# Optimization experiments

Measured on AMD Instinct MI355X. Metric: run time of the kernel, lower is better.

Reference implementation:

```python
import jax, jax.numpy as jnp
import numpy as np

HEADS = 8
DIM_HEAD = 64
RMS_EPS = 1.1920929e-07  # torch default eps = finfo(fp32).eps


def rotate_half(x):
    x1, x2 = jnp.split(x, 2, axis=-1)
    return jnp.concatenate((-x2, x1), axis=-1)


def setup_inputs() -> dict:
    key = jax.random.key(0)
    k1, k2, k3, k4, k5 = jax.random.split(key, 5)
    b, n, dim = 2, 4096, 1024
    dim_hidden = HEADS * DIM_HEAD  # 512
    x = jax.random.normal(k1, (b, n, dim), dtype=jnp.float32)
    rotary_emb = jax.random.normal(k2, (n, DIM_HEAD), dtype=jnp.float32)
    rms_weight = jnp.ones((dim,), dtype=jnp.float32)
    w_qkv = jax.random.normal(k3, (dim, dim_hidden * 3), dtype=jnp.float32) * (dim ** -0.5)
    w_out = jax.random.normal(k4, (dim_hidden, dim), dtype=jnp.float32) * (dim_hidden ** -0.5)
    return {"x": x, "rotary_emb": rotary_emb, "rms_weight": rms_weight,
            "w_qkv": w_qkv, "w_out": w_out}


def reference(x, rotary_emb, rms_weight, w_qkv, w_out):
    b, n, dim = x.shape
    h, d = HEADS, DIM_HEAD
    # RMSNorm
    xn = x * jax.lax.rsqrt(jnp.mean(x * x, axis=-1, keepdims=True) + RMS_EPS) * rms_weight
    # QKV projection, rearrange 'b n (qkv h d) -> qkv b h n d'
    qkv = (xn @ w_qkv).reshape(b, n, 3, h, d).transpose(2, 0, 3, 1, 4)
    q, k, v = qkv[0], qkv[1], qkv[2]
    # RoPE
    cos, sin = jnp.cos(rotary_emb), jnp.sin(rotary_emb)  # (n, d) broadcasts over b,h
    q = q * cos + rotate_half(q) * sin
    k = k * cos + rotate_half(k) * sin
    q = q * (d ** -0.5)
    sim = jnp.einsum('bhid,bhjd->bhij', q, k)
    causal_mask = jnp.triu(jnp.ones((n, n), dtype=bool), 1)
    sim = jnp.where(causal_mask, -jnp.finfo(sim.dtype).max, sim)
    attn = jax.nn.softmax(sim, axis=-1)
    out = jnp.einsum('bhij,bhjd->bhid', attn, v)
    out = out.transpose(0, 2, 1, 3).reshape(b, n, h * d)  # 'b h n d -> b n (h d)'
    return out @ w_out
```

## Files before the change

### kernel.cpp

```cpp
#include <hip/hip_runtime.h>
#include <hip/hip_bf16.h>
#include <cstdint>

using bf16x8 = __attribute__((ext_vector_type(8))) __bf16;
using f32x4  = __attribute__((ext_vector_type(4))) float;

#define LOG2E 1.4426950408889634f

__device__ inline void gload16(__bf16* lds, const __bf16* g) {
    __builtin_amdgcn_global_load_lds((const __attribute__((address_space(1))) void*)g,
                                     (__attribute__((address_space(3))) void*)lds, 16, 0, 0);
}
__device__ inline void wait_barrier4() {
    asm volatile("s_waitcnt vmcnt(4)" ::: "memory");
    __builtin_amdgcn_s_barrier();
}
__device__ inline void wait_barrier0() {
    asm volatile("s_waitcnt vmcnt(0)" ::: "memory");
    __builtin_amdgcn_s_barrier();
}

__global__ __launch_bounds__(256) void prep_kernel(const float* __restrict__ x,
                                                   const float* __restrict__ rmsw,
                                                   __bf16* __restrict__ xn,
                                                   const float* __restrict__ wqkv,
                                                   __bf16* __restrict__ wqkvt,
                                                   const float* __restrict__ wout,
                                                   __bf16* __restrict__ woutt,
                                                   const float* __restrict__ rot,
                                                   uint* __restrict__ csb) {
    __shared__ float tile[32][33];
    __shared__ float part[4];
    const int bid = blockIdx.x;
    const int tid = threadIdx.x;
    if (bid < 8192) {
        const float4 v = reinterpret_cast<const float4*>(x + (size_t)bid * 1024)[tid];
        float ss = v.x * v.x + v.y * v.y + v.z * v.z + v.w * v.w;
#pragma unroll
        for (int i = 1; i < 64; i <<= 1) ss += __shfl_xor(ss, i);
        if ((tid & 63) == 0) part[tid >> 6] = ss;
        __syncthreads();
        const float total = part[0] + part[1] + part[2] + part[3];
        const float scale = rsqrtf(total * (1.0f / 1024.0f) + 1.1920929e-07f);
        const float4 wv = reinterpret_cast<const float4*>(rmsw)[tid];
        union { __bf16 h[4]; uint2 u; } pk;
        pk.h[0] = (__bf16)(v.x * scale * wv.x);
        pk.h[1] = (__bf16)(v.y * scale * wv.y);
        pk.h[2] = (__bf16)(v.z * scale * wv.z);
        pk.h[3] = (__bf16)(v.w * scale * wv.w);
        reinterpret_cast<uint2*>(xn + (size_t)bid * 1024)[tid] = pk.u;
    } else if (bid < 10240) {
        const float* in;
        __bf16* out;
        int K, N, bx, by;
        if (bid < 9728) {
            const int i = bid - 8192;
            in = wqkv; out = wqkvt; K = 1024; N = 1536; bx = i % 48; by = i / 48;
        } else {
            const int i = bid - 9728;
            in = wout; out = woutt; K = 512; N = 1024; bx = i % 32; by = i / 32;
        }
        const int tx = tid & 31, ty = tid >> 5;
        const int n0 = bx * 32, k0 = by * 32;
#pragma unroll
        for (int r = ty; r < 32; r += 8)
            tile[r][tx] = in[(size_t)(k0 + r) * N + n0 + tx];
        __syncthreads();
#pragma unroll
        for (int r = ty; r < 32; r += 8)
            out[(size_t)(n0 + r) * K + k0 + tx] = (__bf16)tile[tx][r];
    } else {
        const int i = (bid - 10240) * 256 + tid;
        float s, c;
        sincosf(rot[i], &s, &c);
        union { __bf16 h[2]; uint u; } p;
        p.h[0] = (__bf16)c;
        p.h[1] = (__bf16)s;
        csb[i] = p.u;
    }
}

__global__ __launch_bounds__(256) void rope_k_kernel(__bf16* __restrict__ qk,
                                                     const uint* __restrict__ csb) {
    const int row = blockIdx.x * 4 + (threadIdx.x >> 6);
    const int lane = threadIdx.x & 63;
    const int h = lane >> 3, dl = (lane & 7) * 4;
    const int pos = row & 4095;
    union { uint4 v; uint u[4]; } A, C;
    A.v = *reinterpret_cast<const uint4*>(csb + pos * 64 + dl);
    C.v = *reinterpret_cast<const uint4*>(csb + pos * 64 + dl + 32);
    __bf16* pp = qk + (size_t)row * 1024 + 512 + h * 64 + dl;
    union { uint2 u; __bf16 hh[4]; } va, vb, oa, ob;
    va.u = *reinterpret_cast<const uint2*>(pp);
    vb.u = *reinterpret_cast<const uint2*>(pp + 32);
#pragma unroll
    for (int j = 0; j < 4; ++j) {
        const float c0 = __uint_as_float(A.u[j] << 16);
        const float s0 = __uint_as_float(A.u[j] & 0xffff0000u);
        const float c1 = __uint_as_float(C.u[j] << 16);
        const float s1 = __uint_as_float(C.u[j] & 0xffff0000u);
        const float a = (float)va.hh[j], b2 = (float)vb.hh[j];
        oa.hh[j] = (__bf16)(a * c0 - b2 * s0);
        ob.hh[j] = (__bf16)(b2 * c1 + a * s1);
    }
    *reinterpret_cast<uint2*>(pp)      = oa.u;
    *reinterpret_cast<uint2*>(pp + 32) = ob.u;
}

__global__ __launch_bounds__(256) void gemm_qkv(const __bf16* __restrict__ A,
                                                const __bf16* __restrict__ Bt,
                                                __bf16* __restrict__ qk,
                                                __bf16* __restrict__ vt) {
    __shared__ __align__(16) __bf16 As[3][128 * 32];
    __shared__ __align__(16) __bf16 Bs[3][128 * 32];
    const int K = 1024, nbn = 12;
    const int xcd = blockIdx.x & 7;
    const int idx = blockIdx.x >> 3;
    const int bm = xcd * 8 + idx / nbn;
    const int bn = idx % nbn;
    const int tid = threadIdx.x;
    const int w = tid >> 6, l = tid & 63, lg = l >> 4, lr = l & 15;
    const int wr = w >> 1, wc = w & 1;
    const __bf16* Ab = A + (size_t)(bm * 128) * K;
    const __bf16* Bb = Bt + (size_t)(bn * 128) * K;
    const int srow = tid >> 2, scol = (tid & 3) * 8;
    const __bf16* Asrc = Ab + (size_t)srow * K + scol;
    const __bf16* Bsrc = Bb + (size_t)srow * K + scol;

    auto stage = [&](int k2) {
        const int nx = k2 % 3;
        const int off = k2 * 32;
        gload16(&As[nx][tid * 8],        Asrc + off);
        gload16(&As[nx][2048 + tid * 8], Asrc + (size_t)64 * K + off);
        gload16(&Bs[nx][tid * 8],        Bsrc + off);
        gload16(&Bs[nx][2048 + tid * 8], Bsrc + (size_t)64 * K + off);
    };

    const int NS = K >> 5;
    f32x4 acc[4][4] = {};
    stage(0);
    stage(1);
    wait_barrier4();

    if (bn < 8) {
        for (int k = 0; k < NS; ++k) {
            const bool more = (k + 2 < NS);
            if (more) stage(k + 2);
            const __bf16* Ac = &As[k % 3][0];
            const __bf16* Bc = &Bs[k % 3][0];
            bf16x8 af[4], bfr[4];
#pragma unroll
            for (int m = 0; m < 4; ++m)
                af[m] = *reinterpret_cast<const bf16x8*>(Ac + (wr * 64 + m * 16 + lr) * 32 + lg * 8);
#pragma unroll
            for (int nn = 0; nn < 4; ++nn)
                bfr[nn] = *reinterpret_cast<const bf16x8*>(Bc + (wc * 64 + nn * 16 + lr) * 32 + lg * 8);
#pragma unroll
            for (int m = 0; m < 4; ++m)
#pragma unroll
                for (int nn = 0; nn < 4; ++nn)
                    acc[m][nn] = __builtin_amdgcn_mfma_f32_16x16x32_bf16(bfr[m], af[nn],
                                                                         acc[m][nn], 0, 0, 0);
            if (more) wait_barrier4();
            else      wait_barrier0();
        }
        const int cb = bn * 128 + wc * 64;
#pragma unroll
        for (int m = 0; m < 4; ++m) {
            const int col = cb + m * 16 + 4 * lg;
#pragma unroll
            for (int nn = 0; nn < 4; ++nn) {
                const int row = bm * 128 + wr * 64 + nn * 16 + lr;
                union { __bf16 h4[4]; uint2 u; } ob;
#pragma unroll
                for (int r = 0; r < 4; ++r) ob.h4[r] = (__bf16)acc[m][nn][r];
                *reinterpret_cast<uint2*>(qk + (size_t)row * 1024 + col) = ob.u;
            }
        }
    } else {
        for (int k = 0; k < NS; ++k) {
            const bool more = (k + 2 < NS);
            if (more) stage(k + 2);
            const __bf16* Ac = &As[k % 3][0];
            const __bf16* Bc = &Bs[k % 3][0];
            bf16x8 af[4], bfr[4];
#pragma unroll
            for (int m = 0; m < 4; ++m)
                af[m] = *reinterpret_cast<const bf16x8*>(Ac + (wr * 64 + m * 16 + lr) * 32 + lg * 8);
#pragma unroll
            for (int nn = 0; nn < 4; ++nn)
                bfr[nn] = *reinterpret_cast<const bf16x8*>(Bc + (wc * 64 + nn * 16 + lr) * 32 + lg * 8);
#pragma unroll
            for (int m = 0; m < 4; ++m)
#pragma unroll
                for (int nn = 0; nn < 4; ++nn)
                    acc[m][nn] = __builtin_amdgcn_mfma_f32_16x16x32_bf16(af[m], bfr[nn],
                                                                         acc[m][nn], 0, 0, 0);
            if (more) wait_barrier4();
            else      wait_barrier0();
        }
        const int cb = bn * 128 + wc * 64;
#pragma unroll
        for (int m = 0; m < 4; ++m) {
            const int rg = bm * 128 + wr * 64 + m * 16 + 4 * lg;
            const int bidx = rg >> 12, pos0 = rg & 4095;
            const int a0 = pos0 & 63;
            const int cp = 32 * (a0 >> 5) + 8 * ((a0 >> 2) & 3) + 4 * ((a0 >> 4) & 1);
            const int nbase = (pos0 & ~63) + cp;
#pragma unroll
            for (int nn = 0; nn < 4; ++nn) {
                const int col = cb + nn * 16 + lr - 1024;
                const int hh = col >> 6, dd = col & 63;
                union { __bf16 h4[4]; uint2 u; } pk2;
#pragma unroll
                for (int r = 0; r < 4; ++r) pk2.h4[r] = (__bf16)acc[m][nn][r];
                *reinterpret_cast<uint2*>(&vt[((size_t)(bidx * 8 + hh) * 64 + dd) * 4096 + nbase]) = pk2.u;
            }
        }
    }
}

__global__ __launch_bounds__(256) void gemm_out(const __bf16* __restrict__ A,
                                                const __bf16* __restrict__ Bt,
                                                float* __restrict__ C) {
    __shared__ __align__(16) __bf16 As[3][128 * 32];
    __shared__ __align__(16) __bf16 Bs[3][128 * 32];
    const int K = 512, N = 1024, nbn = 8;
    const int xcd = blockIdx.x & 7;
    const int idx = blockIdx.x >> 3;
    const int bm = xcd * 8 + idx / nbn;
    const int bn = idx % nbn;
    const int tid = threadIdx.x;
    const int w = tid >> 6, l = tid & 63, lg = l >> 4, lr = l & 15;
    const int wr = w >> 1, wc = w & 1;
    const __bf16* Ab = A + (size_t)(bm * 128) * K;
    const __bf16* Bb = Bt + (size_t)(bn * 128) * K;
    const int srow = tid >> 2, scol = (tid & 3) * 8;
    const __bf16* Asrc = Ab + (size_t)srow * K + scol;
    const __bf16* Bsrc = Bb + (size_t)srow * K + scol;

    auto stage = [&](int k2) {
        const int nx = k2 % 3;
        const int off = k2 * 32;
        gload16(&As[nx][tid * 8],        Asrc + off);
        gload16(&As[nx][2048 + tid * 8], Asrc + (size_t)64 * K + off);
        gload16(&Bs[nx][tid * 8],        Bsrc + off);
        gload16(&Bs[nx][2048 + tid * 8], Bsrc + (size_t)64 * K + off);
    };

    const int NS = K >> 5;
    f32x4 acc[4][4] = {};
    stage(0);
    stage(1);
    wait_barrier4();
    for (int k = 0; k < NS; ++k) {
        const bool more = (k + 2 < NS);
        if (more) stage(k + 2);
        const __bf16* Ac = &As[k % 3][0];
        const __bf16* Bc = &Bs[k % 3][0];
        bf16x8 af[4], bfr[4];
#pragma unroll
        for (int m = 0; m < 4; ++m)
            af[m] = *reinterpret_cast<const bf16x8*>(Ac + (wr * 64 + m * 16 + lr) * 32 + lg * 8);
#pragma unroll
        for (int nn = 0; nn < 4; ++nn)
            bfr[nn] = *reinterpret_cast<const bf16x8*>(Bc + (wc * 64 + nn * 16 + lr) * 32 + lg * 8);
#pragma unroll
        for (int m = 0; m < 4; ++m)
#pragma unroll
            for (int nn = 0; nn < 4; ++nn)
                acc[m][nn] = __builtin_amdgcn_mfma_f32_16x16x32_bf16(bfr[m], af[nn],
                                                                     acc[m][nn], 0, 0, 0);
        if (more) wait_barrier4();
        else      wait_barrier0();
    }
#pragma unroll
    for (int m = 0; m < 4; ++m) {
        const int col = bn * 128 + wc * 64 + m * 16 + 4 * lg;
#pragma unroll
        for (int nn = 0; nn < 4; ++nn) {
            const int row = bm * 128 + wr * 64 + nn * 16 + lr;
            *reinterpret_cast<float4*>(&C[(size_t)row * N + col]) =
                *reinterpret_cast<const float4*>(&acc[m][nn]);
        }
    }
}

__global__ __launch_bounds__(256) void attn_kernel(const __bf16* __restrict__ qkp,
                                                   const __bf16* __restrict__ vt,
                                                   const uint* __restrict__ csb,
                                                   __bf16* __restrict__ attn_out) {
    const int bid = blockIdx.x;
    const int j = bid >> 3;
    const int bh = 2 * (bid & 7) + (j & 1);
    const int qt = 63 - (j >> 1);
    const int b = bh >> 3, h = bh & 7;
    const int tid = threadIdx.x;
    const int w = tid >> 6, l = tid & 63, lg = l >> 4, lr = l & 15;

    __shared__ __align__(16) __bf16 Ks[2][64 * 64];
    __shared__ __align__(16) __bf16 Vs[3][64 * 64];

    const __bf16* qbase = qkp + (size_t)b * 4096 * 1024 + h * 64;
    const __bf16* kbase = qbase + 512;
    const __bf16* vtb   = vt + (size_t)(b * 8 + h) * 64 * 4096;

    const int sr = tid >> 3;
    const int sc = ((tid & 7) ^ (sr & 7)) * 8;
    const __bf16* kp = kbase + (size_t)sr * 1024 + sc;
    const __bf16* vp = vtb + (size_t)sr * 4096 + sc;

    const int xel = (lr & 7) * 8;

    const int wq0 = qt * 64 + 16 * w;
    const int nkt = qt + 1;

    auto stage2 = [&](__bf16* kdst, __bf16* vdst) {
        gload16(kdst + tid * 8,         kp);
        gload16(kdst + (tid + 256) * 8, kp + 32 * 1024);
        gload16(vdst + tid * 8,         vp);
        gload16(vdst + (tid + 256) * 8, vp + 32 * 4096);
        kp += 64 * 1024;
        vp += 64;
    };

    stage2(Ks[0], Vs[0]);
    stage2(Ks[1], Vs[1]);

    bf16x8 Qf[2];
    {
        const __bf16* qp = qbase + (size_t)(wq0 + lr) * 1024 + 8 * lg;
        const bf16x8 rq0 = *reinterpret_cast<const bf16x8*>(qp);
        const bf16x8 rq1 = *reinterpret_cast<const bf16x8*>(qp + 32);
        const uint* csp = csb + (size_t)(wq0 + lr) * 64 + 8 * lg;
        union { uint4 q[2]; uint u[8]; } W0, W1;
        W0.q[0] = *reinterpret_cast<const uint4*>(csp);
        W0.q[1] = *reinterpret_cast<const uint4*>(csp + 4);
        W1.q[0] = *reinterpret_cast<const uint4*>(csp + 32);
        W1.q[1] = *reinterpret_cast<const uint4*>(csp + 36);
        const float qs = 0.125f * LOG2E;
#pragma unroll
        for (int i = 0; i < 8; ++i) {
            const float cax = __uint_as_float(W0.u[i] << 16);
            const float cay = __uint_as_float(W0.u[i] & 0xffff0000u);
            const float cbx = __uint_as_float(W1.u[i] << 16);
            const float cby = __uint_as_float(W1.u[i] & 0xffff0000u);
            const float a = (float)rq0[i], b2 = (float)rq1[i];
            Qf[0][i] = (__bf16)((a * cax - b2 * cay) * qs);
            Qf[1][i] = (__bf16)((b2 * cbx + a * cby) * qs);
        }
    }

    bf16x8 ones;
#pragma unroll
    for (int i = 0; i < 8; ++i) ones[i] = (__bf16)1.0f;

    f32x4 O[4] = {};
    f32x4 Lacc = {};
    float m_ = -1e30f;

    auto qk_step = [&](f32x4 (&S)[4], const __bf16* kb) {
        __builtin_amdgcn_s_setprio(1);
#pragma unroll
        for (int jt = 0; jt < 4; ++jt) {
            const __bf16* kr = kb + (16 * jt + lr) * 64;
            const bf16x8 Kf0 = *reinterpret_cast<const bf16x8*>(kr + ((8 * lg) ^ xel));
            const bf16x8 Kf1 = *reinterpret_cast<const bf16x8*>(kr + ((32 + 8 * lg) ^ xel));
            f32x4 z = {};
            z = __builtin_amdgcn_mfma_f32_16x16x32_bf16(Kf0, Qf[0], z, 0, 0, 0);
            S[jt] = __builtin_amdgcn_mfma_f32_16x16x32_bf16(Kf1, Qf[1], z, 0, 0, 0);
        }
        __builtin_amdgcn_s_setprio(0);
    };
    auto smpv = [&](f32x4 (&SC)[4], const __bf16* vb, bool domask) {
        if (domask) {
#pragma unroll
            for (int jt = 0; jt < 4; ++jt)
#pragma unroll
                for (int r = 0; r < 4; ++r)
                    if (16 * jt + 4 * lg + r > 16 * w + lr) SC[jt][r] = -1e30f;
        }
        float mx = -1e30f;
#pragma unroll
        for (int jt = 0; jt < 4; ++jt)
            mx = fmaxf(mx, fmaxf(fmaxf(SC[jt][0], SC[jt][1]), fmaxf(SC[jt][2], SC[jt][3])));
        if (__any(mx > m_ + 8.0f)) {
            mx = fmaxf(mx, __shfl_xor(mx, 16));
            mx = fmaxf(mx, __shfl_xor(mx, 32));
            const float mn = fmaxf(m_, mx);
            const float alpha = __builtin_amdgcn_exp2f(m_ - mn);
            m_ = mn;
            Lacc *= alpha;
#pragma unroll
            for (int dt = 0; dt < 4; ++dt) O[dt] *= alpha;
        }
#pragma unroll
        for (int jt = 0; jt < 4; ++jt)
#pragma unroll
            for (int r = 0; r < 4; ++r)
                SC[jt][r] = __builtin_amdgcn_exp2f(SC[jt][r] - m_);
        __builtin_amdgcn_s_setprio(1);
#pragma unroll
        for (int s = 0; s < 2; ++s) {
            bf16x8 Pf;
#pragma unroll
            for (int i = 0; i < 8; ++i)
                Pf[i] = (__bf16)SC[2 * s + (i >> 2)][i & 3];
            Lacc = __builtin_amdgcn_mfma_f32_16x16x32_bf16(ones, Pf, Lacc, 0, 0, 0);
#pragma unroll
            for (int dt = 0; dt < 4; ++dt) {
                const bf16x8 Vf = *reinterpret_cast<const bf16x8*>(
                    vb + (16 * dt + lr) * 64 + ((32 * s + 8 * lg) ^ xel));
                O[dt] = __builtin_amdgcn_mfma_f32_16x16x32_bf16(Vf, Pf, O[dt], 0, 0, 0);
            }
        }
        __builtin_amdgcn_s_setprio(0);
    };

    f32x4 S0[4], S1[4];
    int t = 0;

    __syncthreads();
    qk_step(S0, Ks[0]);
    __syncthreads();

    for (; t + 8 <= nkt; t += 6) {
        stage2(Ks[0], Vs[2]); qk_step(S1, Ks[1]); smpv(S0, Vs[0], false); __syncthreads();
        stage2(Ks[1], Vs[0]); qk_step(S0, Ks[0]); smpv(S1, Vs[1], false); __syncthreads();
        stage2(Ks[0], Vs[1]); qk_step(S1, Ks[1]); smpv(S0, Vs[2], false); __syncthreads();
        stage2(Ks[1], Vs[2]); qk_step(S0, Ks[0]); smpv(S1, Vs[0], false); __syncthreads();
        stage2(Ks[0], Vs[0]); qk_step(S1, Ks[1]); smpv(S0, Vs[1], false); __syncthreads();
        stage2(Ks[1], Vs[1]); qk_step(S0, Ks[0]); smpv(S1, Vs[2], false); __syncthreads();
    }

    {
        f32x4 Sp[4];
#pragma unroll
        for (int jt = 0; jt < 4; ++jt) Sp[jt] = S0[jt];
        for (; t < nkt; ++t) {
            if (t + 2 < nkt) stage2(Ks[(t + 2) & 1], Vs[(t + 2) % 3]);
            f32x4 Sn[4];
            if (t + 1 < nkt) qk_step(Sn, Ks[(t + 1) & 1]);
            smpv(Sp, Vs[t % 3], t == nkt - 1);
            __syncthreads();
#pragma unroll
            for (int jt = 0; jt < 4; ++jt) Sp[jt] = Sn[jt];
        }
    }

    const float inv = 1.0f / Lacc[0];
    __bf16* op = attn_out + ((size_t)b * 4096 + wq0 + lr) * 512 + h * 64;
#pragma unroll
    for (int dt = 0; dt < 4; ++dt) {
        union { __bf16 h4[4]; uint2 u; } ow;
#pragma unroll
        for (int r = 0; r < 4; ++r) ow.h4[r] = (__bf16)(O[dt][r] * inv);
        *reinterpret_cast<uint2*>(op + 16 * dt + 4 * lg) = ow.u;
    }
}

extern "C" void kernel_launch(void* const* d_in, const int* in_sizes, int n_in,
                              void* d_out, int out_size, void* d_ws, size_t ws_size,
                              hipStream_t stream) {
    (void)in_sizes; (void)n_in; (void)out_size; (void)ws_size;
    const float* x    = (const float*)d_in[0];
    const float* rot  = (const float*)d_in[1];
    const float* rmsw = (const float*)d_in[2];
    const float* wqkv = (const float*)d_in[3];
    const float* wout = (const float*)d_in[4];
    float* out = (float*)d_out;

    char* ws = (char*)d_ws;
    __bf16* xn    = (__bf16*)ws;
    __bf16* wqkvt = (__bf16*)(ws + 16777216);
    __bf16* woutt = (__bf16*)(ws + 16777216 + 3145728);
    __bf16* aout  = (__bf16*)(ws + 16777216 + 3145728 + 1048576);
    __bf16* qk  = (__bf16*)d_out;
    uint* csb   = (uint*)((char*)d_out + 16777216);
    __bf16* vt  = (__bf16*)((char*)d_out + 18874368);

    prep_kernel<<<11264, 256, 0, stream>>>(x, rmsw, xn, wqkv, wqkvt, wout, woutt, rot, csb);
    gemm_qkv<<<768, 256, 0, stream>>>(xn, wqkvt, qk, vt);
    rope_k_kernel<<<2048, 256, 0, stream>>>(qk, csb);
    attn_kernel<<<1024, 256, 0, stream>>>(qk, vt, csb, aout);
    gemm_out<<<512, 256, 0, stream>>>(aout, woutt, out);
}
```

Before: 130.4 us.

## Fuse RoPE and query scaling into QKV GEMM epilogue, drop rope kernel

Applies the rotary embedding to both Q and K, plus the softmax scale on Q, directly in the QKV GEMM epilogue. It pairs accumulator tiles m and m+2, which hold dims d and d+32 of the same head. This removes the separate rope_k kernel launch and its read-modify-write pass over K, and removes the per-block RoPE work on Q in the attention kernel. The cost is extra cos/sin table loads and arithmetic in the GEMM epilogue, and it depends on the tile-to-head column mapping being correct.

Measured after the change: 124.6 us. 4.4% less time.

```diff
diff --git a/kernel.cpp b/kernel.cpp
--- a/kernel.cpp
+++ b/kernel.cpp
@@ -80,35 +80,9 @@
     }
 }
 
-__global__ __launch_bounds__(256) void rope_k_kernel(__bf16* __restrict__ qk,
-                                                     const uint* __restrict__ csb) {
-    const int row = blockIdx.x * 4 + (threadIdx.x >> 6);
-    const int lane = threadIdx.x & 63;
-    const int h = lane >> 3, dl = (lane & 7) * 4;
-    const int pos = row & 4095;
-    union { uint4 v; uint u[4]; } A, C;
-    A.v = *reinterpret_cast<const uint4*>(csb + pos * 64 + dl);
-    C.v = *reinterpret_cast<const uint4*>(csb + pos * 64 + dl + 32);
-    __bf16* pp = qk + (size_t)row * 1024 + 512 + h * 64 + dl;
-    union { uint2 u; __bf16 hh[4]; } va, vb, oa, ob;
-    va.u = *reinterpret_cast<const uint2*>(pp);
-    vb.u = *reinterpret_cast<const uint2*>(pp + 32);
-#pragma unroll
-    for (int j = 0; j < 4; ++j) {
-        const float c0 = __uint_as_float(A.u[j] << 16);
-        const float s0 = __uint_as_float(A.u[j] & 0xffff0000u);
-        const float c1 = __uint_as_float(C.u[j] << 16);
-        const float s1 = __uint_as_float(C.u[j] & 0xffff0000u);
-        const float a = (float)va.hh[j], b2 = (float)vb.hh[j];
-        oa.hh[j] = (__bf16)(a * c0 - b2 * s0);
-        ob.hh[j] = (__bf16)(b2 * c1 + a * s1);
-    }
-    *reinterpret_cast<uint2*>(pp)      = oa.u;
-    *reinterpret_cast<uint2*>(pp + 32) = ob.u;
-}
-
 __global__ __launch_bounds__(256) void gemm_qkv(const __bf16* __restrict__ A,
                                                 const __bf16* __restrict__ Bt,
+                                                const uint* __restrict__ csb,
                                                 __bf16* __restrict__ qk,
                                                 __bf16* __restrict__ vt) {
     __shared__ __align__(16) __bf16 As[3][128 * 32];
@@ -165,16 +139,32 @@
             else      wait_barrier0();
         }
         const int cb = bn * 128 + wc * 64;
-#pragma unroll
-        for (int m = 0; m < 4; ++m) {
-            const int col = cb + m * 16 + 4 * lg;
-#pragma unroll
-            for (int nn = 0; nn < 4; ++nn) {
-                const int row = bm * 128 + wr * 64 + nn * 16 + lr;
-                union { __bf16 h4[4]; uint2 u; } ob;
-#pragma unroll
-                for (int r = 0; r < 4; ++r) ob.h4[r] = (__bf16)acc[m][nn][r];
-                *reinterpret_cast<uint2*>(qk + (size_t)row * 1024 + col) = ob.u;
+        const float sc = (cb < 512) ? 0.125f * LOG2E : 1.0f;
+#pragma unroll
+        for (int nn = 0; nn < 4; ++nn) {
+            const int row = bm * 128 + wr * 64 + nn * 16 + lr;
+            const int pos = row & 4095;
+            const uint* csp = csb + pos * 64 + 4 * lg;
+            __bf16* qrow = qk + (size_t)row * 1024 + cb + 4 * lg;
+#pragma unroll
+            for (int m = 0; m < 2; ++m) {
+                union { uint4 v; uint u[4]; } Wlo, Whi;
+                Wlo.v = *reinterpret_cast<const uint4*>(csp + m * 16);
+                Whi.v = *reinterpret_cast<const uint4*>(csp + m * 16 + 32);
+                union { __bf16 h4[4]; uint2 u; } lo, hi;
+#pragma unroll
+                for (int r = 0; r < 4; ++r) {
+                    const float c0 = __uint_as_float(Wlo.u[r] << 16);
+                    const float s0 = __uint_as_float(Wlo.u[r] & 0xffff0000u);
+                    const float c1 = __uint_as_float(Whi.u[r] << 16);
+                    const float s1 = __uint_as_float(Whi.u[r] & 0xffff0000u);
+                    const float a  = acc[m][nn][r];
+                    const float b2 = acc[m + 2][nn][r];
+                    lo.h4[r] = (__bf16)((a * c0 - b2 * s0) * sc);
+                    hi.h4[r] = (__bf16)((b2 * c1 + a * s1) * sc);
+                }
+                *reinterpret_cast<uint2*>(qrow + m * 16)      = lo.u;
+                *reinterpret_cast<uint2*>(qrow + m * 16 + 32) = hi.u;
             }
         }
     } else {
@@ -288,7 +278,6 @@
 
 __global__ __launch_bounds__(256) void attn_kernel(const __bf16* __restrict__ qkp,
                                                    const __bf16* __restrict__ vt,
-                                                   const uint* __restrict__ csb,
                                                    __bf16* __restrict__ attn_out) {
     const int bid = blockIdx.x;
     const int j = bid >> 3;
@@ -330,25 +319,8 @@
     bf16x8 Qf[2];
     {
         const __bf16* qp = qbase + (size_t)(wq0 + lr) * 1024 + 8 * lg;
-        const bf16x8 rq0 = *reinterpret_cast<const bf16x8*>(qp);
-        const bf16x8 rq1 = *reinterpret_cast<const bf16x8*>(qp + 32);
-        const uint* csp = csb + (size_t)(wq0 + lr) * 64 + 8 * lg;
-        union { uint4 q[2]; uint u[8]; } W0, W1;
-        W0.q[0] = *reinterpret_cast<const uint4*>(csp);
-        W0.q[1] = *reinterpret_cast<const uint4*>(csp + 4);
-        W1.q[0] = *reinterpret_cast<const uint4*>(csp + 32);
-        W1.q[1] = *reinterpret_cast<const uint4*>(csp + 36);
-        const float qs = 0.125f * LOG2E;
-#pragma unroll
-        for (int i = 0; i < 8; ++i) {
-            const float cax = __uint_as_float(W0.u[i] << 16);
-            const float cay = __uint_as_float(W0.u[i] & 0xffff0000u);
-            const float cbx = __uint_as_float(W1.u[i] << 16);
-            const float cby = __uint_as_float(W1.u[i] & 0xffff0000u);
-            const float a = (float)rq0[i], b2 = (float)rq1[i];
-            Qf[0][i] = (__bf16)((a * cax - b2 * cay) * qs);
-            Qf[1][i] = (__bf16)((b2 * cbx + a * cby) * qs);
-        }
+        Qf[0] = *reinterpret_cast<const bf16x8*>(qp);
+        Qf[1] = *reinterpret_cast<const bf16x8*>(qp + 32);
     }
 
     bf16x8 ones;
@@ -480,8 +452,7 @@
     __bf16* vt  = (__bf16*)((char*)d_out + 18874368);
 
     prep_kernel<<<11264, 256, 0, stream>>>(x, rmsw, xn, wqkv, wqkvt, wout, woutt, rot, csb);
-    gemm_qkv<<<768, 256, 0, stream>>>(xn, wqkvt, qk, vt);
-    rope_k_kernel<<<2048, 256, 0, stream>>>(qk, csb);
-    attn_kernel<<<1024, 256, 0, stream>>>(qk, vt, csb, aout);
+    gemm_qkv<<<768, 256, 0, stream>>>(xn, wqkvt, csb, qk, vt);
+    attn_kernel<<<1024, 256, 0, stream>>>(qk, vt, aout);
     gemm_out<<<512, 256, 0, stream>>>(aout, woutt, out);
 }
```
